# Optimization experiments

Hardware: AMD Instinct MI355X
Metric: run time of the kernel (lower is better)

## Reference

```python
import jax, jax.numpy as jnp
import numpy as np

H = 16
D_MODEL = 1024
D_K = D_MODEL // H  # 64
NEG = -1e9


def setup_inputs() -> dict:
    key = jax.random.key(0)
    ks = jax.random.split(key, 9)
    nb, nw = 4, 2048
    Q = jax.random.normal(ks[0], (nb, nw, D_MODEL), dtype=jnp.float32)
    K = jax.random.normal(ks[1], (nb, nw, D_MODEL), dtype=jnp.float32)
    V = jax.random.normal(ks[2], (nb, nw, D_MODEL), dtype=jnp.float32)
    mask = jax.random.randint(ks[3], (nb, nw, nw), 0, 2, dtype=jnp.int32)
    s = 1.0 / np.sqrt(D_MODEL)
    Wq = jax.random.normal(ks[4], (D_MODEL, D_MODEL), dtype=jnp.float32) * s
    Wk = jax.random.normal(ks[5], (D_MODEL, D_MODEL), dtype=jnp.float32) * s
    Wv = jax.random.normal(ks[6], (D_MODEL, D_MODEL), dtype=jnp.float32) * s
    Wo = jax.random.normal(ks[7], (D_MODEL, D_MODEL), dtype=jnp.float32) * s
    return {"Q": Q, "K": K, "V": V, "mask": mask,
            "Wq": Wq, "Wk": Wk, "Wv": Wv, "Wo": Wo}


def reference(Q, K, V, mask, Wq, Wk, Wv, Wo):
    nb, nw, _ = Q.shape
    scaling = jnp.asarray(np.sqrt(D_K), dtype=Q.dtype)
    # nn.Linear(bias=False): y = x @ W.T; split heads -> [nb, h, nw, d_k]
    q = (Q @ Wq.T).reshape(nb, nw, H, D_K).transpose(0, 2, 1, 3)
    k = (K @ Wk.T).reshape(nb, nw, H, D_K).transpose(0, 2, 1, 3)
    v = (V @ Wv.T).reshape(nb, nw, H, D_K).transpose(0, 2, 1, 3)
    scores = jnp.einsum('bhqd,bhkd->bhqk', q, k) / scaling
    # mask broadcast over heads (unsqueeze(1) in torch)
    scores = jnp.where(mask[:, None, :, :] == 0, jnp.asarray(NEG, scores.dtype), scores)
    probs = jax.nn.softmax(scores, axis=-1)
    # dropout is identity in eval mode
    attn = jnp.einsum('bhqk,bhkd->bhqd', probs, v)
    x = attn.transpose(0, 2, 1, 3).reshape(nb, nw, D_MODEL)
    return x @ Wo.T
```

## Files before the change

### kernel.cpp

```cpp
#include <hip/hip_runtime.h>
#include <hip/hip_bf16.h>
#include <cstdint>
#include <cmath>

#define NB 4
#define NW 2048
#define DM 1024
#define NH 16
#define DK 64

typedef __attribute__((ext_vector_type(8))) short bf16x8;
typedef __attribute__((ext_vector_type(4))) float f32x4;
union cvt8 { uint4 u; __hip_bfloat16 h[8]; };
union pk2 { unsigned u; unsigned short s[2]; };

__device__ __forceinline__ void async_ld16(const void* g, void* l) {
  __builtin_amdgcn_global_load_lds((__attribute__((address_space(1))) void*)g,
                                   (__attribute__((address_space(3))) void*)l,
                                   16, 0, 0);
}

__device__ __forceinline__ unsigned short bf16bits(float x) {
  __hip_bfloat16 h = __float2bfloat16(x);
  return *(unsigned short*)&h;
}

__device__ __forceinline__ float exp2_fast(float x) {
  float r;
  asm("v_exp_f32 %0, %1" : "=v"(r) : "v"(x));
  return r;
}

__global__ void __launch_bounds__(256) cvt_qkv(const float* __restrict__ Q,
                                               const float* __restrict__ K,
                                               const float* __restrict__ V,
                                               __hip_bfloat16* __restrict__ Qb,
                                               __hip_bfloat16* __restrict__ Kb,
                                               __hip_bfloat16* __restrict__ Vb) {
  const float* in = blockIdx.y == 0 ? Q : (blockIdx.y == 1 ? K : V);
  __hip_bfloat16* out = blockIdx.y == 0 ? Qb : (blockIdx.y == 1 ? Kb : Vb);
  size_t i = ((size_t)blockIdx.x * 256 + threadIdx.x) * 8;
  float4 a = *(const float4*)(in + i);
  float4 b = *(const float4*)(in + i + 4);
  cvt8 c;
#pragma unroll
  for (int t = 0; t < 4; ++t) {
    c.h[t]     = __float2bfloat16(((const float*)&a)[t]);
    c.h[4 + t] = __float2bfloat16(((const float*)&b)[t]);
  }
  *(uint4*)(out + i) = c.u;
}

__global__ void __launch_bounds__(256) cvt_w(const float* __restrict__ W0,
                                             const float* __restrict__ W1,
                                             const float* __restrict__ W2,
                                             const float* __restrict__ W3,
                                             __hip_bfloat16* __restrict__ Wb) {
  const float* in = blockIdx.y == 0 ? W0 : (blockIdx.y == 1 ? W1 : (blockIdx.y == 2 ? W2 : W3));
  __hip_bfloat16* out = Wb + (size_t)blockIdx.y * DM * DM;
  size_t i = ((size_t)blockIdx.x * 256 + threadIdx.x) * 8;
  float4 a = *(const float4*)(in + i);
  float4 b = *(const float4*)(in + i + 4);
  cvt8 c;
#pragma unroll
  for (int t = 0; t < 4; ++t) {
    c.h[t]     = __float2bfloat16(((const float*)&a)[t]);
    c.h[4 + t] = __float2bfloat16(((const float*)&b)[t]);
  }
  *(uint4*)(out + i) = c.u;
}

__global__ void __launch_bounds__(256) mask_pack(const int* __restrict__ mask,
                                                 unsigned long long* __restrict__ bits) {
  int lane = threadIdx.x & 63;
  size_t tid = (size_t)blockIdx.x * blockDim.x + threadIdx.x;
  size_t widx = tid >> 6;
  int m = mask[widx * 64 + lane];
  unsigned long long bm = __ballot(m != 0);
  if (lane == 0) {
    int kt  = (int)(widx & 31);
    int row = (int)((widx >> 5) & 2047);
    int bb  = (int)(widx >> 16);
    bits[((size_t)bb * 32 + kt) * NW + row] = bm;
  }
}

__global__ void __launch_bounds__(256) gemm_qkv(const __hip_bfloat16* __restrict__ Qb,
                                                const __hip_bfloat16* __restrict__ Kb,
                                                const __hip_bfloat16* __restrict__ Vb,
                                                const __hip_bfloat16* __restrict__ Wb,
                                                __hip_bfloat16* __restrict__ q_ws,
                                                __hip_bfloat16* __restrict__ k_ws,
                                                __hip_bfloat16* __restrict__ vt) {
  __shared__ __align__(16) __hip_bfloat16 sA[128 * 32];
  __shared__ __align__(16) __hip_bfloat16 sB[128 * 32];
  const int z = blockIdx.z;
  const __hip_bfloat16* A = z == 0 ? Qb : (z == 1 ? Kb : Vb);
  const __hip_bfloat16* W = Wb + (size_t)z * DM * DM;
  const int tid = threadIdx.x;
  const int lane = tid & 63;
  const int l15 = lane & 15, quad = lane >> 4;
  const int rowA = blockIdx.y * 128;
  const int colB = blockIdx.x * 128;
  const int wm = ((tid >> 6) >> 1) * 64, wn = ((tid >> 6) & 1) * 64;

  const f32x4 fz = {0.f, 0.f, 0.f, 0.f};
  f32x4 acc[4][4];
#pragma unroll
  for (int i = 0; i < 4; ++i)
#pragma unroll
    for (int j = 0; j < 4; ++j) acc[i][j] = fz;

  for (int k0 = 0; k0 < DM; k0 += 32) {
#pragma unroll
    for (int j = 0; j < 2; ++j) {
      int c = j * 256 + tid;
      int r = c >> 2, col = (c & 3) * 8;
      int ldsOff = (j * 256 + (tid & ~63)) * 16;
      async_ld16(A + (size_t)(rowA + r) * DM + k0 + col, (char*)sA + ldsOff);
      async_ld16(W + (size_t)(colB + r) * DM + k0 + col, (char*)sB + ldsOff);
    }
    __syncthreads();
    bf16x8 af[4], bfr[4];
#pragma unroll
    for (int i = 0; i < 4; ++i) {
      af[i]  = *(const bf16x8*)(sA + (wm + i * 16 + l15) * 32 + quad * 8);
      bfr[i] = *(const bf16x8*)(sB + (wn + i * 16 + l15) * 32 + quad * 8);
    }
#pragma unroll
    for (int i = 0; i < 4; ++i)
#pragma unroll
      for (int j = 0; j < 4; ++j)
        acc[i][j] = __builtin_amdgcn_mfma_f32_16x16x32_bf16(af[i], bfr[j], acc[i][j], 0, 0, 0);
    __syncthreads();
  }

  if (z < 2) {
    __hip_bfloat16* C = z == 0 ? q_ws : k_ws;
    float alpha = z == 0 ? 0.18033688011112042f : 1.0f;
#pragma unroll
    for (int i = 0; i < 4; ++i) {
      int row = rowA + wm + i * 16 + quad * 4;
#pragma unroll
      for (int j = 0; j < 4; ++j) {
        int col = colB + wn + j * 16 + l15;
#pragma unroll
        for (int r = 0; r < 4; ++r)
          C[(size_t)(row + r) * DM + col] = __float2bfloat16(acc[i][j][r] * alpha);
      }
    }
  } else {
#pragma unroll
    for (int i = 0; i < 4; ++i) {
      int row = rowA + wm + i * 16 + quad * 4;
      int bb = row >> 11, tok = row & 2047;
#pragma unroll
      for (int j = 0; j < 4; ++j) {
        int col = colB + wn + j * 16 + l15;
        uint2 u;
        u.x = (unsigned int)bf16bits(acc[i][j][0]) | ((unsigned int)bf16bits(acc[i][j][1]) << 16);
        u.y = (unsigned int)bf16bits(acc[i][j][2]) | ((unsigned int)bf16bits(acc[i][j][3]) << 16);
        *(uint2*)(vt + ((size_t)bb * 1024 + col) * 2048 + tok) = u;
      }
    }
  }
}

__global__ void __launch_bounds__(256) gemm_out(const __hip_bfloat16* __restrict__ A,
                                                const __hip_bfloat16* __restrict__ W,
                                                float* __restrict__ C) {
  __shared__ __align__(16) __hip_bfloat16 sA[128 * 32];
  __shared__ __align__(16) __hip_bfloat16 sB[128 * 32];
  const int tid = threadIdx.x;
  const int lane = tid & 63;
  const int l15 = lane & 15, quad = lane >> 4;
  const int rowA = blockIdx.y * 128;
  const int colB = blockIdx.x * 128;
  const int wm = ((tid >> 6) >> 1) * 64, wn = ((tid >> 6) & 1) * 64;

  const f32x4 fz = {0.f, 0.f, 0.f, 0.f};
  f32x4 acc[4][4];
#pragma unroll
  for (int i = 0; i < 4; ++i)
#pragma unroll
    for (int j = 0; j < 4; ++j) acc[i][j] = fz;

  for (int k0 = 0; k0 < DM; k0 += 32) {
#pragma unroll
    for (int j = 0; j < 2; ++j) {
      int c = j * 256 + tid;
      int r = c >> 2, col = (c & 3) * 8;
      int ldsOff = (j * 256 + (tid & ~63)) * 16;
      async_ld16(A + (size_t)(rowA + r) * DM + k0 + col, (char*)sA + ldsOff);
      async_ld16(W + (size_t)(colB + r) * DM + k0 + col, (char*)sB + ldsOff);
    }
    __syncthreads();
    bf16x8 af[4], bfr[4];
#pragma unroll
    for (int i = 0; i < 4; ++i) {
      af[i]  = *(const bf16x8*)(sA + (wm + i * 16 + l15) * 32 + quad * 8);
      bfr[i] = *(const bf16x8*)(sB + (wn + i * 16 + l15) * 32 + quad * 8);
    }
#pragma unroll
    for (int i = 0; i < 4; ++i)
#pragma unroll
      for (int j = 0; j < 4; ++j)
        acc[i][j] = __builtin_amdgcn_mfma_f32_16x16x32_bf16(af[i], bfr[j], acc[i][j], 0, 0, 0);
    __syncthreads();
  }
#pragma unroll
  for (int i = 0; i < 4; ++i) {
    int row = rowA + wm + i * 16 + quad * 4;
#pragma unroll
    for (int j = 0; j < 4; ++j) {
      int col = colB + wn + j * 16 + l15;
#pragma unroll
      for (int r = 0; r < 4; ++r)
        C[(size_t)(row + r) * DM + col] = acc[i][j][r];
    }
  }
}

#define LDSK 72

__global__ void __launch_bounds__(256) attn_fused(const __hip_bfloat16* __restrict__ q,
                                                  const __hip_bfloat16* __restrict__ kk,
                                                  const __hip_bfloat16* __restrict__ vt,
                                                  const unsigned long long* __restrict__ mbt,
                                                  __hip_bfloat16* __restrict__ o) {
  __shared__ __align__(16) __hip_bfloat16 sK[64 * LDSK];
  __shared__ __align__(16) __hip_bfloat16 sVT[64 * LDSK];

  const int tid = threadIdx.x;
  const int wave = tid >> 6, lane = tid & 63;
  const int l15 = lane & 15, quad = lane >> 4;
  const int b = blockIdx.z, h = blockIdx.y;
  const int qbase = blockIdx.x * 128 + wave * 32;

  const __hip_bfloat16* qp = q + (size_t)(b * NW + qbase + l15) * DM + h * DK + quad * 8;
  bf16x8 aq0 = *(const bf16x8*)qp;
  bf16x8 aq1 = *(const bf16x8*)(qp + 32);
  bf16x8 aq2 = *(const bf16x8*)(qp + (size_t)16 * DM);
  bf16x8 aq3 = *(const bf16x8*)(qp + (size_t)16 * DM + 32);

  const __hip_bfloat16* vbase = vt + ((size_t)b * 1024 + h * DK) * 2048;
  const unsigned long long* mrow = mbt + (size_t)b * 32 * NW + qbase + l15;

  const f32x4 fz = {0.f, 0.f, 0.f, 0.f};
  f32x4 oacc[2][4];
#pragma unroll
  for (int g = 0; g < 2; ++g)
#pragma unroll
    for (int i = 0; i < 4; ++i) oacc[g][i] = fz;
  float lsr0[4] = {0.f, 0.f, 0.f, 0.f};
  float lsr1[4] = {0.f, 0.f, 0.f, 0.f};

  for (int kt = 0; kt < NW / 64; ++kt) {
    __syncthreads();
#pragma unroll
    for (int j = 0; j < 2; ++j) {
      int c = j * 256 + tid;
      int r = c >> 3, col = (c & 7) * 8;
      *(uint4*)(sK + r * LDSK + col) =
          *(const uint4*)(kk + (size_t)(b * NW + kt * 64 + r) * DM + h * DK + col);
      *(uint4*)(sVT + r * LDSK + col) =
          *(const uint4*)(vbase + (size_t)r * 2048 + kt * 64 + col);
    }
    unsigned long long mw0 = mrow[(size_t)kt * NW];
    unsigned long long mw1 = mrow[(size_t)kt * NW + 16];
    __syncthreads();

    unsigned long long msh0 = mw0 >> (quad * 4);
    unsigned long long msh1 = mw1 >> (quad * 4);
    unsigned u0[4][2], u1[4][2];
#pragma unroll
    for (int nc = 0; nc < 4; ++nc) {
      bf16x8 kf0 = *(const bf16x8*)(sK + (nc * 16 + l15) * LDSK + quad * 8);
      bf16x8 kf1 = *(const bf16x8*)(sK + (nc * 16 + l15) * LDSK + 32 + quad * 8);
      f32x4 t0 = fz, t1 = fz;
      t0 = __builtin_amdgcn_mfma_f32_16x16x32_bf16(kf0, aq0, t0, 0, 0, 0);
      t0 = __builtin_amdgcn_mfma_f32_16x16x32_bf16(kf1, aq1, t0, 0, 0, 0);
      t1 = __builtin_amdgcn_mfma_f32_16x16x32_bf16(kf0, aq2, t1, 0, 0, 0);
      t1 = __builtin_amdgcn_mfma_f32_16x16x32_bf16(kf1, aq3, t1, 0, 0, 0);
      unsigned nib0 = (unsigned)(msh0 >> (nc * 16)) & 0xFu;
      unsigned nib1 = (unsigned)(msh1 >> (nc * 16)) & 0xFu;
      float p0[4], p1[4];
#pragma unroll
      for (int r = 0; r < 4; ++r) {
        float e0 = exp2_fast(t0[r]);
        float e1 = exp2_fast(t1[r]);
        if (!((nib0 >> r) & 1u)) e0 = 0.f;
        if (!((nib1 >> r) & 1u)) e1 = 0.f;
        lsr0[r] += e0;
        lsr1[r] += e1;
        p0[r] = e0;
        p1[r] = e1;
      }
      pk2 w;
      w.s[0] = bf16bits(p0[0]); w.s[1] = bf16bits(p0[1]); u0[nc][0] = w.u;
      w.s[0] = bf16bits(p0[2]); w.s[1] = bf16bits(p0[3]); u0[nc][1] = w.u;
      w.s[0] = bf16bits(p1[0]); w.s[1] = bf16bits(p1[1]); u1[nc][0] = w.u;
      w.s[0] = bf16bits(p1[2]); w.s[1] = bf16bits(p1[3]); u1[nc][1] = w.u;
    }

#define PERM2(x, y)                                                  \
    asm volatile("v_permlane32_swap_b32 %0, %1" : "+v"(x), "+v"(y)); \
    asm volatile("v_permlane16_swap_b32 %0, %1" : "+v"(x), "+v"(y));
    unsigned g0a0 = u0[0][0], g0a2 = u0[1][0]; PERM2(g0a0, g0a2)
    unsigned g0a1 = u0[0][1], g0a3 = u0[1][1]; PERM2(g0a1, g0a3)
    unsigned g0c0 = u0[2][0], g0c2 = u0[3][0]; PERM2(g0c0, g0c2)
    unsigned g0c1 = u0[2][1], g0c3 = u0[3][1]; PERM2(g0c1, g0c3)
    unsigned g1a0 = u1[0][0], g1a2 = u1[1][0]; PERM2(g1a0, g1a2)
    unsigned g1a1 = u1[0][1], g1a3 = u1[1][1]; PERM2(g1a1, g1a3)
    unsigned g1c0 = u1[2][0], g1c2 = u1[3][0]; PERM2(g1c0, g1c2)
    unsigned g1c1 = u1[2][1], g1c3 = u1[3][1]; PERM2(g1c1, g1c3)
#undef PERM2

    union { unsigned w[4]; bf16x8 v; } A00, A01, A10, A11;
    A00.w[0] = g0a0; A00.w[1] = g0a1; A00.w[2] = g0a2; A00.w[3] = g0a3;
    A01.w[0] = g0c0; A01.w[1] = g0c1; A01.w[2] = g0c2; A01.w[3] = g0c3;
    A10.w[0] = g1a0; A10.w[1] = g1a1; A10.w[2] = g1a2; A10.w[3] = g1a3;
    A11.w[0] = g1c0; A11.w[1] = g1c1; A11.w[2] = g1c2; A11.w[3] = g1c3;

#pragma unroll
    for (int nc = 0; nc < 4; ++nc) {
      bf16x8 vf0 = *(const bf16x8*)(sVT + (nc * 16 + l15) * LDSK + quad * 8);
      bf16x8 vf1 = *(const bf16x8*)(sVT + (nc * 16 + l15) * LDSK + 32 + quad * 8);
      oacc[0][nc] = __builtin_amdgcn_mfma_f32_16x16x32_bf16(A00.v, vf0, oacc[0][nc], 0, 0, 0);
      oacc[0][nc] = __builtin_amdgcn_mfma_f32_16x16x32_bf16(A01.v, vf1, oacc[0][nc], 0, 0, 0);
      oacc[1][nc] = __builtin_amdgcn_mfma_f32_16x16x32_bf16(A10.v, vf0, oacc[1][nc], 0, 0, 0);
      oacc[1][nc] = __builtin_amdgcn_mfma_f32_16x16x32_bf16(A11.v, vf1, oacc[1][nc], 0, 0, 0);
    }
  }

  float ls0 = (lsr0[0] + lsr0[1]) + (lsr0[2] + lsr0[3]);
  ls0 += __shfl_xor(ls0, 16, 64);
  ls0 += __shfl_xor(ls0, 32, 64);
  float ls1 = (lsr1[0] + lsr1[1]) + (lsr1[2] + lsr1[3]);
  ls1 += __shfl_xor(ls1, 16, 64);
  ls1 += __shfl_xor(ls1, 32, 64);

  float inv0[4], inv1[4];
#pragma unroll
  for (int r = 0; r < 4; ++r) {
    float lv0 = __shfl(ls0, quad * 4 + r, 64);
    float lv1 = __shfl(ls1, quad * 4 + r, 64);
    inv0[r] = 1.0f / fmaxf(lv0, 1e-30f);
    inv1[r] = 1.0f / fmaxf(lv1, 1e-30f);
  }
#pragma unroll
  for (int nc = 0; nc < 4; ++nc)
#pragma unroll
    for (int r = 0; r < 4; ++r) {
      o[(size_t)(b * NW + qbase + quad * 4 + r) * DM + h * DK + nc * 16 + l15] =
          __float2bfloat16(oacc[0][nc][r] * inv0[r]);
      o[(size_t)(b * NW + qbase + 16 + quad * 4 + r) * DM + h * DK + nc * 16 + l15] =
          __float2bfloat16(oacc[1][nc][r] * inv1[r]);
    }
}

extern "C" void kernel_launch(void* const* d_in, const int* in_sizes, int n_in,
                              void* d_out, int out_size, void* d_ws, size_t ws_size,
                              hipStream_t stream) {
  const float* Q  = (const float*)d_in[0];
  const float* K  = (const float*)d_in[1];
  const float* V  = (const float*)d_in[2];
  const int*   Mm = (const int*)d_in[3];
  const float* Wq = (const float*)d_in[4];
  const float* Wk = (const float*)d_in[5];
  const float* Wv = (const float*)d_in[6];
  const float* Wo = (const float*)d_in[7];
  float* out = (float*)d_out;

  char* ws = (char*)d_ws;
  const size_t tb = (size_t)NB * NW * DM * sizeof(__hip_bfloat16);
  const size_t wb = (size_t)DM * DM * sizeof(__hip_bfloat16);
  __hip_bfloat16* Qb   = (__hip_bfloat16*)(ws);
  __hip_bfloat16* Kb   = (__hip_bfloat16*)(ws + tb);
  __hip_bfloat16* k_ws = (__hip_bfloat16*)(ws + 2 * tb);
  __hip_bfloat16* vt   = (__hip_bfloat16*)(ws + 3 * tb);
  __hip_bfloat16* Wb   = (__hip_bfloat16*)(ws + 4 * tb);
  unsigned long long* mbits = (unsigned long long*)(ws + 4 * tb + 4 * wb);
  __hip_bfloat16* q_ws = (__hip_bfloat16*)d_out;
  __hip_bfloat16* Vb   = (__hip_bfloat16*)((char*)d_out + tb);
  __hip_bfloat16* a_ws = Qb;

  const int gq = (int)((size_t)NB * NW * DM / 8 / 256);
  const int gw = (int)((size_t)DM * DM / 8 / 256);

  mask_pack<<<(size_t)NB * NW * NW / 256, 256, 0, stream>>>(Mm, mbits);
  cvt_qkv<<<dim3(gq, 3), 256, 0, stream>>>(Q, K, V, Qb, Kb, Vb);
  cvt_w<<<dim3(gw, 4), 256, 0, stream>>>(Wq, Wk, Wv, Wo, Wb);
  gemm_qkv<<<dim3(DM / 128, NB * NW / 128, 3), 256, 0, stream>>>(Qb, Kb, Vb, Wb,
                                                                 q_ws, k_ws, vt);
  attn_fused<<<dim3(NW / 128, NH, NB), 256, 0, stream>>>(q_ws, k_ws, vt, mbits, a_ws);
  gemm_out<<<dim3(DM / 128, NB * NW / 128), 256, 0, stream>>>(a_ws, Wb + 3 * (size_t)DM * DM, out);
}
```

Before: 495.4 us.

## Double-buffer K/V tiles in LDS with register prefetch in attention loop

The fused attention kernel now keeps two LDS buffers for K and V^T. It loads the next tile's K, V and mask words from global memory into registers before computing the current tile, then writes them to the other buffer after the PV MFMAs. This hides global load latency behind compute and cuts the loop from two barriers to one. The cost is double LDS use and more registers, which may lower occupancy.

```diff
diff --git a/kernel.cpp b/kernel.cpp
--- a/kernel.cpp
+++ b/kernel.cpp
@@ -228,8 +228,8 @@
                                                   const __hip_bfloat16* __restrict__ vt,
                                                   const unsigned long long* __restrict__ mbt,
                                                   __hip_bfloat16* __restrict__ o) {
-  __shared__ __align__(16) __hip_bfloat16 sK[64 * LDSK];
-  __shared__ __align__(16) __hip_bfloat16 sVT[64 * LDSK];
+  __shared__ __align__(16) __hip_bfloat16 sK[2 * 64 * LDSK];
+  __shared__ __align__(16) __hip_bfloat16 sVT[2 * 64 * LDSK];
 
   const int tid = threadIdx.x;
   const int wave = tid >> 6, lane = tid & 63;
@@ -246,6 +246,10 @@
   const __hip_bfloat16* vbase = vt + ((size_t)b * 1024 + h * DK) * 2048;
   const unsigned long long* mrow = mbt + (size_t)b * 32 * NW + qbase + l15;
 
+  const int r0 = tid >> 3, scol = (tid & 7) * 8;
+  const __hip_bfloat16* kst = kk + (size_t)(b * NW + r0) * DM + h * DK + scol;
+  const __hip_bfloat16* vst = vbase + (size_t)r0 * 2048 + scol;
+
   const f32x4 fz = {0.f, 0.f, 0.f, 0.f};
   f32x4 oacc[2][4];
 #pragma unroll
@@ -255,28 +259,39 @@
   float lsr0[4] = {0.f, 0.f, 0.f, 0.f};
   float lsr1[4] = {0.f, 0.f, 0.f, 0.f};
 
+  uint4 stk0 = *(const uint4*)(kst);
+  uint4 stk1 = *(const uint4*)(kst + (size_t)32 * DM);
+  uint4 stv0 = *(const uint4*)(vst);
+  uint4 stv1 = *(const uint4*)(vst + (size_t)32 * 2048);
+  unsigned long long mw0 = mrow[0];
+  unsigned long long mw1 = mrow[16];
+  *(uint4*)(sK + r0 * LDSK + scol) = stk0;
+  *(uint4*)(sK + (r0 + 32) * LDSK + scol) = stk1;
+  *(uint4*)(sVT + r0 * LDSK + scol) = stv0;
+  *(uint4*)(sVT + (r0 + 32) * LDSK + scol) = stv1;
+  __syncthreads();
+
   for (int kt = 0; kt < NW / 64; ++kt) {
-    __syncthreads();
-#pragma unroll
-    for (int j = 0; j < 2; ++j) {
-      int c = j * 256 + tid;
-      int r = c >> 3, col = (c & 7) * 8;
-      *(uint4*)(sK + r * LDSK + col) =
-          *(const uint4*)(kk + (size_t)(b * NW + kt * 64 + r) * DM + h * DK + col);
-      *(uint4*)(sVT + r * LDSK + col) =
-          *(const uint4*)(vbase + (size_t)r * 2048 + kt * 64 + col);
-    }
-    unsigned long long mw0 = mrow[(size_t)kt * NW];
-    unsigned long long mw1 = mrow[(size_t)kt * NW + 16];
-    __syncthreads();
-
-    unsigned long long msh0 = mw0 >> (quad * 4);
-    unsigned long long msh1 = mw1 >> (quad * 4);
+    const __hip_bfloat16* bK = sK + (kt & 1) * (64 * LDSK);
+    const __hip_bfloat16* bV = sVT + (kt & 1) * (64 * LDSK);
+    const unsigned long long cmw0 = mw0, cmw1 = mw1;
+    const bool notlast = (kt + 1 < NW / 64);
+    if (notlast) {
+      stk0 = *(const uint4*)(kst + (size_t)(kt + 1) * 64 * DM);
+      stk1 = *(const uint4*)(kst + (size_t)(kt + 1) * 64 * DM + (size_t)32 * DM);
+      stv0 = *(const uint4*)(vst + (kt + 1) * 64);
+      stv1 = *(const uint4*)(vst + (kt + 1) * 64 + (size_t)32 * 2048);
+      mw0 = mrow[(size_t)(kt + 1) * NW];
+      mw1 = mrow[(size_t)(kt + 1) * NW + 16];
+    }
+
+    unsigned long long msh0 = cmw0 >> (quad * 4);
+    unsigned long long msh1 = cmw1 >> (quad * 4);
     unsigned u0[4][2], u1[4][2];
 #pragma unroll
     for (int nc = 0; nc < 4; ++nc) {
-      bf16x8 kf0 = *(const bf16x8*)(sK + (nc * 16 + l15) * LDSK + quad * 8);
-      bf16x8 kf1 = *(const bf16x8*)(sK + (nc * 16 + l15) * LDSK + 32 + quad * 8);
+      bf16x8 kf0 = *(const bf16x8*)(bK + (nc * 16 + l15) * LDSK + quad * 8);
+      bf16x8 kf1 = *(const bf16x8*)(bK + (nc * 16 + l15) * LDSK + 32 + quad * 8);
       f32x4 t0 = fz, t1 = fz;
       t0 = __builtin_amdgcn_mfma_f32_16x16x32_bf16(kf0, aq0, t0, 0, 0, 0);
       t0 = __builtin_amdgcn_mfma_f32_16x16x32_bf16(kf1, aq1, t0, 0, 0, 0);
@@ -324,12 +339,22 @@
 
 #pragma unroll
     for (int nc = 0; nc < 4; ++nc) {
-      bf16x8 vf0 = *(const bf16x8*)(sVT + (nc * 16 + l15) * LDSK + quad * 8);
-      bf16x8 vf1 = *(const bf16x8*)(sVT + (nc * 16 + l15) * LDSK + 32 + quad * 8);
+      bf16x8 vf0 = *(const bf16x8*)(bV + (nc * 16 + l15) * LDSK + quad * 8);
+      bf16x8 vf1 = *(const bf16x8*)(bV + (nc * 16 + l15) * LDSK + 32 + quad * 8);
       oacc[0][nc] = __builtin_amdgcn_mfma_f32_16x16x32_bf16(A00.v, vf0, oacc[0][nc], 0, 0, 0);
       oacc[0][nc] = __builtin_amdgcn_mfma_f32_16x16x32_bf16(A01.v, vf1, oacc[0][nc], 0, 0, 0);
       oacc[1][nc] = __builtin_amdgcn_mfma_f32_16x16x32_bf16(A10.v, vf0, oacc[1][nc], 0, 0, 0);
       oacc[1][nc] = __builtin_amdgcn_mfma_f32_16x16x32_bf16(A11.v, vf1, oacc[1][nc], 0, 0, 0);
+    }
+
+    if (notlast) {
+      __hip_bfloat16* nK = sK + ((kt + 1) & 1) * (64 * LDSK);
+      __hip_bfloat16* nV = sVT + ((kt + 1) & 1) * (64 * LDSK);
+      *(uint4*)(nK + r0 * LDSK + scol) = stk0;
+      *(uint4*)(nK + (r0 + 32) * LDSK + scol) = stk1;
+      *(uint4*)(nV + r0 * LDSK + scol) = stv0;
+      *(uint4*)(nV + (r0 + 32) * LDSK + scol) = stv1;
+      __syncthreads();
     }
   }
 
```

New measurement: 447.1 us. 1.11x faster.

## Double-buffer K/V tiles in attention with async global-to-LDS loads and XOR swizzle

Applied to the files above, without the earlier changes.

The attention kernel now keeps two LDS buffers for the K and V^T tiles and prefetches the next tile with global_load_lds while computing on the current one. The mask words are also prefetched a tile ahead. The padded layout is replaced by an XOR-swizzled 64-wide layout, because async direct-to-LDS loads cannot write padded rows, and the swizzle is meant to avoid bank conflicts. This drops one barrier per iteration and hides global latency, at the cost of doubling LDS use and relying on the single barrier to order the async writes.

```diff
diff --git a/kernel.cpp b/kernel.cpp
--- a/kernel.cpp
+++ b/kernel.cpp
@@ -221,15 +221,13 @@
   }
 }
 
-#define LDSK 72
-
 __global__ void __launch_bounds__(256) attn_fused(const __hip_bfloat16* __restrict__ q,
                                                   const __hip_bfloat16* __restrict__ kk,
                                                   const __hip_bfloat16* __restrict__ vt,
                                                   const unsigned long long* __restrict__ mbt,
                                                   __hip_bfloat16* __restrict__ o) {
-  __shared__ __align__(16) __hip_bfloat16 sK[64 * LDSK];
-  __shared__ __align__(16) __hip_bfloat16 sVT[64 * LDSK];
+  __shared__ __align__(16) __hip_bfloat16 sK[2 * 64 * 64];
+  __shared__ __align__(16) __hip_bfloat16 sVT[2 * 64 * 64];
 
   const int tid = threadIdx.x;
   const int wave = tid >> 6, lane = tid & 63;
@@ -246,6 +244,12 @@
   const __hip_bfloat16* vbase = vt + ((size_t)b * 1024 + h * DK) * 2048;
   const unsigned long long* mrow = mbt + (size_t)b * 32 * NW + qbase + l15;
 
+  const int sgran = (tid & 7) ^ ((tid >> 3) & 7);
+  const int Rbase = wave * 16 + ((tid >> 3) & 7);
+  const __hip_bfloat16* kst = kk + (size_t)(b * NW + Rbase) * DM + h * DK + sgran * 8;
+  const __hip_bfloat16* vst = vbase + (size_t)Rbase * 2048 + sgran * 8;
+  const int ldsWoff = wave * 2048;
+
   const f32x4 fz = {0.f, 0.f, 0.f, 0.f};
   f32x4 oacc[2][4];
 #pragma unroll
@@ -255,28 +259,41 @@
   float lsr0[4] = {0.f, 0.f, 0.f, 0.f};
   float lsr1[4] = {0.f, 0.f, 0.f, 0.f};
 
+  async_ld16(kst,                     (char*)sK + ldsWoff);
+  async_ld16(kst + (size_t)8 * DM,    (char*)sK + ldsWoff + 1024);
+  async_ld16(vst,                     (char*)sVT + ldsWoff);
+  async_ld16(vst + (size_t)8 * 2048,  (char*)sVT + ldsWoff + 1024);
+  unsigned long long mw0 = mrow[0];
+  unsigned long long mw1 = mrow[16];
+  __syncthreads();
+
+  const int xg = l15 & 7;
+
   for (int kt = 0; kt < NW / 64; ++kt) {
-    __syncthreads();
-#pragma unroll
-    for (int j = 0; j < 2; ++j) {
-      int c = j * 256 + tid;
-      int r = c >> 3, col = (c & 7) * 8;
-      *(uint4*)(sK + r * LDSK + col) =
-          *(const uint4*)(kk + (size_t)(b * NW + kt * 64 + r) * DM + h * DK + col);
-      *(uint4*)(sVT + r * LDSK + col) =
-          *(const uint4*)(vbase + (size_t)r * 2048 + kt * 64 + col);
-    }
-    unsigned long long mw0 = mrow[(size_t)kt * NW];
-    unsigned long long mw1 = mrow[(size_t)kt * NW + 16];
-    __syncthreads();
-
-    unsigned long long msh0 = mw0 >> (quad * 4);
-    unsigned long long msh1 = mw1 >> (quad * 4);
+    const __hip_bfloat16* bK = sK + (kt & 1) * 4096;
+    const __hip_bfloat16* bV = sVT + (kt & 1) * 4096;
+    const unsigned long long cmw0 = mw0, cmw1 = mw1;
+    const bool notlast = (kt + 1 < NW / 64);
+    if (notlast) {
+      int boff = ((kt + 1) & 1) * 8192;
+      const __hip_bfloat16* kn = kst + (size_t)(kt + 1) * 64 * DM;
+      const __hip_bfloat16* vn = vst + (size_t)(kt + 1) * 64;
+      async_ld16(kn,                    (char*)sK + boff + ldsWoff);
+      async_ld16(kn + (size_t)8 * DM,   (char*)sK + boff + ldsWoff + 1024);
+      async_ld16(vn,                    (char*)sVT + boff + ldsWoff);
+      async_ld16(vn + (size_t)8 * 2048, (char*)sVT + boff + ldsWoff + 1024);
+      mw0 = mrow[(size_t)(kt + 1) * NW];
+      mw1 = mrow[(size_t)(kt + 1) * NW + 16];
+    }
+
+    unsigned long long msh0 = cmw0 >> (quad * 4);
+    unsigned long long msh1 = cmw1 >> (quad * 4);
     unsigned u0[4][2], u1[4][2];
 #pragma unroll
     for (int nc = 0; nc < 4; ++nc) {
-      bf16x8 kf0 = *(const bf16x8*)(sK + (nc * 16 + l15) * LDSK + quad * 8);
-      bf16x8 kf1 = *(const bf16x8*)(sK + (nc * 16 + l15) * LDSK + 32 + quad * 8);
+      const __hip_bfloat16* kr = bK + (nc * 16 + l15) * 64;
+      bf16x8 kf0 = *(const bf16x8*)(kr + (quad ^ xg) * 8);
+      bf16x8 kf1 = *(const bf16x8*)(kr + ((quad ^ xg) ^ 4) * 8);
       f32x4 t0 = fz, t1 = fz;
       t0 = __builtin_amdgcn_mfma_f32_16x16x32_bf16(kf0, aq0, t0, 0, 0, 0);
       t0 = __builtin_amdgcn_mfma_f32_16x16x32_bf16(kf1, aq1, t0, 0, 0, 0);
@@ -324,13 +341,16 @@
 
 #pragma unroll
     for (int nc = 0; nc < 4; ++nc) {
-      bf16x8 vf0 = *(const bf16x8*)(sVT + (nc * 16 + l15) * LDSK + quad * 8);
-      bf16x8 vf1 = *(const bf16x8*)(sVT + (nc * 16 + l15) * LDSK + 32 + quad * 8);
+      const __hip_bfloat16* vr = bV + (nc * 16 + l15) * 64;
+      bf16x8 vf0 = *(const bf16x8*)(vr + (quad ^ xg) * 8);
+      bf16x8 vf1 = *(const bf16x8*)(vr + ((quad ^ xg) ^ 4) * 8);
       oacc[0][nc] = __builtin_amdgcn_mfma_f32_16x16x32_bf16(A00.v, vf0, oacc[0][nc], 0, 0, 0);
       oacc[0][nc] = __builtin_amdgcn_mfma_f32_16x16x32_bf16(A01.v, vf1, oacc[0][nc], 0, 0, 0);
       oacc[1][nc] = __builtin_amdgcn_mfma_f32_16x16x32_bf16(A10.v, vf0, oacc[1][nc], 0, 0, 0);
       oacc[1][nc] = __builtin_amdgcn_mfma_f32_16x16x32_bf16(A11.v, vf1, oacc[1][nc], 0, 0, 0);
     }
+
+    if (notlast) __syncthreads();
   }
 
   float ls0 = (lsr0[0] + lsr0[1]) + (lsr0[2] + lsr0[3]);
```

Result: faster. 451.3 us (-8.9%).
